# Optimization experiments

Hardware: AMD Instinct MI355X
Metric: run time of the kernel (lower is better)

## Reference

```python
import jax, jax.numpy as jnp
import numpy as np

N, E, DIN, DH, DOUT = 50000, 800000, 128, 256, 128
EPS = 1e-5
SLOPE = 0.01  # torch leaky_relu default


def setup_inputs() -> dict:
    key = jax.random.key(0)
    ks = jax.random.split(key, 8)
    w = lambda k, shape: jax.random.normal(k, shape, jnp.float32) * 0.05
    return {
        "x": jax.random.normal(ks[0], (N, DIN), jnp.float32),
        "edge_index": jax.random.randint(ks[1], (2, E), 0, N, jnp.int32),
        "W0": w(ks[2], (DH, DIN)),  "b0": jnp.zeros((DH,), jnp.float32),
        "g0": jnp.ones((DH,), jnp.float32), "be0": jnp.zeros((DH,), jnp.float32),
        "W1": w(ks[3], (DH, DH)),   "b1": jnp.zeros((DH,), jnp.float32),
        "g1": jnp.ones((DH,), jnp.float32), "be1": jnp.zeros((DH,), jnp.float32),
        "W2": w(ks[4], (DOUT, DH)), "b2": jnp.zeros((DOUT,), jnp.float32),
        "g2": jnp.ones((DOUT,), jnp.float32), "be2": jnp.zeros((DOUT,), jnp.float32),
    }


def _gcn_forward(x, edge_index, params):
    n = x.shape[0]
    loop = jnp.arange(n, dtype=edge_index.dtype)
    src = jnp.concatenate([edge_index[0], loop])  # add self-loops
    dst = jnp.concatenate([edge_index[1], loop])
    deg = jnp.zeros((n,), x.dtype).at[dst].add(1.0)
    dinv = jax.lax.rsqrt(deg)  # deg >= 1 due to self-loops
    enorm = (dinv[src] * dinv[dst])[:, None]  # [E+N, 1]

    def conv(h, W, b):
        h = h @ W.T  # linear first (PyG GCNConv), messages in out_dim
        msg = h[src] * enorm
        return jax.ops.segment_sum(msg, dst, num_segments=n) + b

    def bn(h, g, be):  # BatchNorm1d, training-mode batch stats (biased var)
        mu = h.mean(0)
        var = ((h - mu) ** 2).mean(0)
        return (h - mu) * jax.lax.rsqrt(var + EPS) * g + be

    (W0, b0, g0, be0, W1, b1, g1, be1, W2, b2, g2, be2) = params
    h = jax.nn.leaky_relu(bn(conv(x, W0, b0), g0, be0), SLOPE)
    h = jax.nn.leaky_relu(bn(conv(h, W1, b1), g1, be1), SLOPE)
    h = bn(conv(h, W2, b2), g2, be2)  # last layer: no leaky_relu
    return h


def reference(x, edge_index, W0, b0, g0, be0, W1, b1, g1, be1, W2, b2, g2, be2):
    return _gcn_forward(x, edge_index,
                        (W0, b0, g0, be0, W1, b1, g1, be1, W2, b2, g2, be2))
```

## Files before the change

kernel.cpp:

```cpp
#include <hip/hip_runtime.h>
#include <hip/hip_bf16.h>

#define N_NODES 50000
#define N_EDGES 800000
#define DIN 128
#define DH   256
#define DOUT 128
#define EPSV 1e-5f
#define SLOPE 0.01f
#define SCAN_NB ((N_NODES + 255) / 256)

typedef __bf16 bf16x8 __attribute__((ext_vector_type(8)));
typedef __bf16 bf16x4 __attribute__((ext_vector_type(4)));
typedef float  f32x4  __attribute__((ext_vector_type(4)));

__global__ void cast3_kernel(const float* __restrict__ W0, const float* __restrict__ W1,
                             const float* __restrict__ W2,
                             __bf16* __restrict__ w0b, __bf16* __restrict__ w1b,
                             __bf16* __restrict__ w2b) {
    constexpr int n0 = DH * DIN / 4, n1 = DH * DH / 4, n2 = DOUT * DH / 4;
    int i = blockIdx.x * blockDim.x + threadIdx.x;
    const float* src; __bf16* dst; int k;
    if (i < n0)           { src = W0; dst = w0b; k = i; }
    else if (i < n0 + n1) { src = W1; dst = w1b; k = i - n0; }
    else if (i < n0 + n1 + n2) { src = W2; dst = w2b; k = i - n0 - n1; }
    else return;
    float4 v = ((const float4*)src)[k];
    bf16x4 o; o[0] = (__bf16)v.x; o[1] = (__bf16)v.y; o[2] = (__bf16)v.z; o[3] = (__bf16)v.w;
    ((bf16x4*)dst)[k] = o;
}

__global__ void cast_scale_kernel(const float* __restrict__ src, const float* __restrict__ dinv,
                                  __bf16* __restrict__ dst) {
    int i = blockIdx.x * blockDim.x + threadIdx.x;
    if (i < N_NODES * (DIN / 8)) {
        int row = i / (DIN / 8);
        float d = dinv[row];
        float4 a = ((const float4*)src)[i * 2];
        float4 b = ((const float4*)src)[i * 2 + 1];
        bf16x8 o;
        o[0] = (__bf16)(a.x * d); o[1] = (__bf16)(a.y * d);
        o[2] = (__bf16)(a.z * d); o[3] = (__bf16)(a.w * d);
        o[4] = (__bf16)(b.x * d); o[5] = (__bf16)(b.y * d);
        o[6] = (__bf16)(b.z * d); o[7] = (__bf16)(b.w * d);
        ((bf16x8*)dst)[i] = o;
    }
}

__global__ void deg_kernel(const int* __restrict__ dst, int* __restrict__ deg) {
    int i = blockIdx.x * blockDim.x + threadIdx.x;
    if (i < N_EDGES) atomicAdd(&deg[dst[i]], 1);
}

__global__ __launch_bounds__(256) void scan_bsum(const int* __restrict__ deg,
                                                 int* __restrict__ bsum,
                                                 float* __restrict__ dinv) {
    __shared__ int lds[256];
    int i = blockIdx.x * 256 + threadIdx.x;
    int dv = 0;
    if (i < N_NODES) {
        dv = deg[i] + 1;
        dinv[i] = rsqrtf((float)dv);
    }
    lds[threadIdx.x] = dv;
    __syncthreads();
    #pragma unroll
    for (int off = 128; off > 0; off >>= 1) {
        if (threadIdx.x < off) lds[threadIdx.x] += lds[threadIdx.x + off];
        __syncthreads();
    }
    if (threadIdx.x == 0) bsum[blockIdx.x] = lds[0];
}

__global__ __launch_bounds__(256) void scan_boffs(const int* __restrict__ bsum,
                                                  int* __restrict__ boffs) {
    __shared__ int lds[256];
    const int t = threadIdx.x;
    lds[t] = (t < SCAN_NB) ? bsum[t] : 0;
    __syncthreads();
    #pragma unroll
    for (int off = 1; off < 256; off <<= 1) {
        int add = (t >= off) ? lds[t - off] : 0;
        __syncthreads();
        lds[t] += add;
        __syncthreads();
    }
    boffs[t] = (t == 0) ? 0 : lds[t - 1];
}

__global__ __launch_bounds__(256) void scan_write(const int* __restrict__ deg,
                                                  const int* __restrict__ boffs,
                                                  int* __restrict__ rp) {
    __shared__ int lds[256];
    const int t = threadIdx.x;
    int i = blockIdx.x * 256 + t;
    int v = (i < N_NODES) ? deg[i] + 1 : 0;
    lds[t] = v;
    __syncthreads();
    #pragma unroll
    for (int off = 1; off < 256; off <<= 1) {
        int add = (t >= off) ? lds[t - off] : 0;
        __syncthreads();
        lds[t] += add;
        __syncthreads();
    }
    if (i < N_NODES) rp[i] = boffs[blockIdx.x] + lds[t] - v;
    if (i == N_NODES - 1) rp[N_NODES] = boffs[blockIdx.x] + lds[t];
}

__global__ void scatter_kernel(const int* __restrict__ ei,
                               const int* __restrict__ rp, int* __restrict__ cursor,
                               int* __restrict__ csr) {
    int e = blockIdx.x * blockDim.x + threadIdx.x;
    if (e >= N_EDGES + N_NODES) return;
    int pos, src;
    if (e < N_EDGES) {
        src = ei[e]; int dst = ei[N_EDGES + e];
        pos = rp[dst] + atomicAdd(&cursor[dst], 1);
    } else {
        src = e - N_EDGES;
        pos = rp[src + 1] - 1;
    }
    csr[pos] = src;
}

template<int C8>
__global__ __launch_bounds__(256) void spmm_b(const int* __restrict__ rp,
                                              const int* __restrict__ csr,
                                              const float* __restrict__ dinv,
                                              const __bf16* __restrict__ h,
                                              __bf16* __restrict__ outp) {
    constexpr int RPB = 256 / C8;
    const int r = blockIdx.x * RPB + threadIdx.x / C8;
    const int l = threadIdx.x % C8;
    if (r >= N_NODES) return;
    const bf16x8* __restrict__ h8 = (const bf16x8*)h;
    const int e0 = rp[r], e1 = rp[r + 1];
    float acc0[8] = {}, acc1[8] = {};
    int e = e0;
    for (; e + 8 <= e1; e += 8) {
        int p[8];
        #pragma unroll
        for (int u = 0; u < 8; ++u) p[u] = csr[e + u];
        bf16x8 v[8];
        #pragma unroll
        for (int u = 0; u < 8; ++u) v[u] = h8[(long)p[u] * C8 + l];
        #pragma unroll
        for (int u = 0; u < 8; ++u) {
            #pragma unroll
            for (int j = 0; j < 8; ++j) {
                if (u & 1) acc1[j] += (float)v[u][j];
                else       acc0[j] += (float)v[u][j];
            }
        }
    }
    for (; e + 2 <= e1; e += 2) {
        int p0 = csr[e], p1 = csr[e + 1];
        bf16x8 v0 = h8[(long)p0 * C8 + l];
        bf16x8 v1 = h8[(long)p1 * C8 + l];
        #pragma unroll
        for (int j = 0; j < 8; ++j) {
            acc0[j] += (float)v0[j];
            acc1[j] += (float)v1[j];
        }
    }
    if (e < e1) {
        int p0 = csr[e];
        bf16x8 v0 = h8[(long)p0 * C8 + l];
        #pragma unroll
        for (int j = 0; j < 8; ++j) acc0[j] += (float)v0[j];
    }
    const float d = dinv[r];
    bf16x8 ob;
    #pragma unroll
    for (int j = 0; j < 8; ++j) ob[j] = (__bf16)((acc0[j] + acc1[j]) * d);
    ((bf16x8*)outp)[(long)r * C8 + l] = ob;
}

template<int K, int NC, bool FUSE_BN, bool RELU, bool SCALE>
__global__ __launch_bounds__(256) void gemm_tile(const __bf16* __restrict__ A,
                                                 const __bf16* __restrict__ W,
                                                 const float* __restrict__ ss,
                                                 const float* __restrict__ dinv,
                                                 __bf16* __restrict__ C,
                                                 int M) {
    constexpr int NW = NC / 64;
    constexpr int MW = 4 / NW;
    constexpr int BM = MW * 64;
    constexpr int NSTEP = K / 32;
    __shared__ __bf16 As[2][BM][40];

    const int tid = threadIdx.x;
    const int wave = tid >> 6, lane = tid & 63;
    const int ln15 = lane & 15, kg = lane >> 4;
    const int wm = wave / NW, wn = wave % NW;
    const int m0 = blockIdx.x * BM;
    const int srow = tid >> 2, schunk = tid & 3;

    int grow[MW];
    #pragma unroll
    for (int p = 0; p < MW; ++p) {
        int gr = m0 + p * 64 + srow;
        grow[p] = gr < M ? gr : M - 1;
    }

    f32x4 acc[4][4];
    #pragma unroll
    for (int i = 0; i < 4; ++i)
        #pragma unroll
        for (int j = 0; j < 4; ++j) acc[i][j] = (f32x4){0.f, 0.f, 0.f, 0.f};

#define LOAD_A(vv, kt_)                                                         \
    _Pragma("unroll")                                                           \
    for (int p = 0; p < MW; ++p)                                                \
        vv[p] = *(const bf16x8*)(A + (long)grow[p] * K + (kt_) + schunk * 8);

#define XFORM_A(vv, kt_)                                                        \
    if (FUSE_BN) {                                                              \
        const f32x4* ss4 = (const f32x4*)ss;                                    \
        int ci = ((kt_) + schunk * 8) >> 2;                                     \
        f32x4 sc0 = ss4[ci],            sc1 = ss4[ci + 1];                      \
        f32x4 sh0 = ss4[(K >> 2) + ci], sh1 = ss4[(K >> 2) + ci + 1];           \
        _Pragma("unroll")                                                       \
        for (int p = 0; p < MW; ++p) {                                          \
            float f[8];                                                         \
            _Pragma("unroll")                                                   \
            for (int j = 0; j < 4; ++j) {                                       \
                f[j]     = fmaf((float)vv[p][j],     sc0[j], sh0[j]);           \
                f[j + 4] = fmaf((float)vv[p][j + 4], sc1[j], sh1[j]);           \
            }                                                                   \
            if (RELU) {                                                         \
                _Pragma("unroll")                                               \
                for (int j = 0; j < 8; ++j) f[j] = f[j] > 0.f ? f[j] : SLOPE * f[j]; \
            }                                                                   \
            _Pragma("unroll")                                                   \
            for (int j = 0; j < 8; ++j) vv[p][j] = (__bf16)f[j];                \
        }                                                                       \
    }

#define WRITE_A(buf, vv)                                                        \
    _Pragma("unroll")                                                           \
    for (int p = 0; p < MW; ++p)                                                \
        *(bf16x8*)(&As[buf][p * 64 + srow][schunk * 8]) = vv[p];

    bf16x8 v0[MW], v[MW];
    LOAD_A(v0, 0)
    XFORM_A(v0, 0)
    WRITE_A(0, v0)
    if (NSTEP > 1) {
        LOAD_A(v, 32)
        XFORM_A(v, 32)
    }
    __syncthreads();

    int cur = 0;
    #pragma unroll
    for (int step = 0; step < NSTEP; ++step) {
        const int kt = step * 32;
        if (step + 1 < NSTEP) {
            WRITE_A(cur ^ 1, v)
        }
        bf16x8 vn[MW];
        if (step + 2 < NSTEP) {
            LOAD_A(vn, kt + 64)
        }
        bf16x8 b[4];
        #pragma unroll
        for (int j = 0; j < 4; ++j)
            b[j] = *(const bf16x8*)(W + (long)(wn * 64 + j * 16 + ln15) * K + kt + kg * 8);
        #pragma unroll
        for (int i = 0; i < 4; ++i) {
            bf16x8 a = *(const bf16x8*)(&As[cur][wm * 64 + i * 16 + ln15][kg * 8]);
            #pragma unroll
            for (int j = 0; j < 4; ++j)
                acc[i][j] = __builtin_amdgcn_mfma_f32_16x16x32_bf16(a, b[j], acc[i][j], 0, 0, 0);
        }
        if (step + 2 < NSTEP) {
            XFORM_A(vn, kt + 64)
            #pragma unroll
            for (int p = 0; p < MW; ++p) v[p] = vn[p];
        }
        __syncthreads();
        cur ^= 1;
    }
#undef LOAD_A
#undef XFORM_A
#undef WRITE_A

    #pragma unroll
    for (int i = 0; i < 4; ++i) {
        #pragma unroll
        for (int q = 0; q < 4; ++q) {
            int r = m0 + wm * 64 + i * 16 + kg * 4 + q;
            if (r < M) {
                float d = SCALE ? dinv[r] : 1.0f;
                #pragma unroll
                for (int j = 0; j < 4; ++j)
                    C[(long)r * NC + wn * 64 + j * 16 + ln15] = (__bf16)(acc[i][j][q] * d);
            }
        }
    }
}

#define NB_STATS 128
template<int C>
__global__ __launch_bounds__(256) void bn_stats(const __bf16* __restrict__ hp,
                                                float* __restrict__ partial) {
    constexpr int LPR = C / 4;
    constexpr int RPI = 256 / LPR;
    const int chunk = threadIdx.x % LPR;
    const int rof   = threadIdx.x / LPR;
    float s[4] = {}, s2[4] = {};
    for (int r = blockIdx.x * RPI + rof; r < N_NODES; r += NB_STATS * RPI) {
        bf16x4 x = ((const bf16x4*)hp)[(long)r * LPR + chunk];
        #pragma unroll
        for (int j = 0; j < 4; ++j) {
            float v = (float)x[j];
            s[j] += v; s2[j] += v * v;
        }
    }
    __shared__ float red[256 * 8];
    #pragma unroll
    for (int j = 0; j < 4; ++j) { red[threadIdx.x * 8 + j] = s[j]; red[threadIdx.x * 8 + 4 + j] = s2[j]; }
    __syncthreads();
    if (rof == 0) {
        #pragma unroll
        for (int g = 1; g < RPI; ++g) {
            #pragma unroll
            for (int j = 0; j < 4; ++j) {
                s[j]  += red[(g * LPR + chunk) * 8 + j];
                s2[j] += red[(g * LPR + chunk) * 8 + 4 + j];
            }
        }
        #pragma unroll
        for (int j = 0; j < 4; ++j) {
            partial[blockIdx.x * 2 * C + chunk * 4 + j]     = s[j];
            partial[blockIdx.x * 2 * C + C + chunk * 4 + j] = s2[j];
        }
    }
}

template<int C>
__global__ __launch_bounds__(1024) void bn_reduce(const float* __restrict__ partial, int nb,
                                                  const float* __restrict__ g,
                                                  const float* __restrict__ be,
                                                  float* __restrict__ ss) {
    constexpr int G = 1024 / C;
    const int c = threadIdx.x % C;
    const int grp = threadIdx.x / C;
    float s = 0.f, q = 0.f;
    for (int b = grp; b < nb; b += G) {
        s += partial[(long)b * 2 * C + c];
        q += partial[(long)b * 2 * C + C + c];
    }
    __shared__ float reds[1024], redq[1024];
    reds[threadIdx.x] = s; redq[threadIdx.x] = q;
    __syncthreads();
    if (grp == 0) {
        #pragma unroll
        for (int gg = 1; gg < G; ++gg) { s += reds[gg * C + c]; q += redq[gg * C + c]; }
        const float invn = 1.0f / (float)N_NODES;
        float mean = s * invn;
        float var  = q * invn - mean * mean;
        float rstd = rsqrtf(var + EPSV);
        float sc = g[c] * rstd;
        ss[c] = sc;
        ss[C + c] = be[c] - mean * sc;
    }
}

template<int C>
__global__ __launch_bounds__(256) void bn_apply_b2f(const __bf16* __restrict__ in,
                                                    float* __restrict__ outp,
                                                    const float* __restrict__ ss) {
    constexpr int LPR = C / 4;
    const long total = (long)N_NODES * LPR;
    const long stride = (long)gridDim.x * blockDim.x;
    for (long idx = (long)blockIdx.x * blockDim.x + threadIdx.x; idx < total; idx += stride) {
        int chunk = (int)(idx % LPR);
        float4 sc = ((const float4*)ss)[chunk];
        float4 sh = ((const float4*)(ss + C))[chunk];
        bf16x4 x = ((const bf16x4*)in)[idx];
        float4 o;
        o.x = fmaf((float)x[0], sc.x, sh.x);
        o.y = fmaf((float)x[1], sc.y, sh.y);
        o.z = fmaf((float)x[2], sc.z, sh.z);
        o.w = fmaf((float)x[3], sc.w, sh.w);
        ((float4*)outp)[idx] = o;
    }
}

extern "C" void kernel_launch(void* const* d_in, const int* in_sizes, int n_in,
                              void* d_out, int out_size, void* d_ws, size_t ws_size,
                              hipStream_t stream) {
    const float* x   = (const float*)d_in[0];
    const int*   ei  = (const int*)  d_in[1];
    const float* W0  = (const float*)d_in[2];
    const float* g0  = (const float*)d_in[4];
    const float* be0 = (const float*)d_in[5];
    const float* W1  = (const float*)d_in[6];
    const float* g1  = (const float*)d_in[8];
    const float* be1 = (const float*)d_in[9];
    const float* W2  = (const float*)d_in[10];
    const float* g2  = (const float*)d_in[12];
    const float* be2 = (const float*)d_in[13];
    float* out = (float*)d_out;

    char* wsb = (char*)d_ws;
    auto alloc = [&](size_t bytes) { char* p = wsb; wsb += (bytes + 255) & ~255UL; return p; };
    int*    deg     = (int*)   alloc(N_NODES * 4);
    int*    cursor  = (int*)   alloc(N_NODES * 4);
    int*    rp      = (int*)   alloc((N_NODES + 4) * 4);
    float*  dinv    = (float*) alloc(N_NODES * 4);
    int*    bsum    = (int*)   alloc(256 * 4);
    int*    boffs   = (int*)   alloc(257 * 4);
    float*  partial = (float*) alloc(NB_STATS * 2 * DH * 4);
    float*  ss      = (float*) alloc(2 * DH * 4);
    int*    csr     = (int*)   alloc((size_t)(N_EDGES + N_NODES) * 4);
    __bf16* w0b     = (__bf16*)alloc(DH * DIN * 2);
    __bf16* w1b     = (__bf16*)alloc(DH * DH * 2);
    __bf16* w2b     = (__bf16*)alloc(DOUT * DH * 2);
    __bf16* xb      = (__bf16*)alloc((size_t)N_NODES * DIN * 2);
    __bf16* bf0     = (__bf16*)alloc((size_t)N_NODES * DH * 2);
    __bf16* bf1     = (__bf16*)alloc((size_t)N_NODES * DH * 2);

    hipMemsetAsync(deg, 0, (size_t)((char*)cursor - (char*)deg) + N_NODES * 4, stream);

    cast3_kernel<<<(DH * DIN / 4 + DH * DH / 4 + DOUT * DH / 4 + 255) / 256, 256, 0, stream>>>(
        W0, W1, W2, w0b, w1b, w2b);

    deg_kernel<<<(N_EDGES + 255) / 256, 256, 0, stream>>>(ei + N_EDGES, deg);
    scan_bsum<<<SCAN_NB, 256, 0, stream>>>(deg, bsum, dinv);
    scan_boffs<<<1, 256, 0, stream>>>(bsum, boffs);
    scan_write<<<SCAN_NB, 256, 0, stream>>>(deg, boffs, rp);
    scatter_kernel<<<(N_EDGES + N_NODES + 255) / 256, 256, 0, stream>>>(ei, rp, cursor, csr);

    cast_scale_kernel<<<(N_NODES * (DIN / 8) + 255) / 256, 256, 0, stream>>>(x, dinv, xb);

    spmm_b<DIN / 8><<<(N_NODES * (DIN / 8) + 255) / 256, 256, 0, stream>>>(
        rp, csr, dinv, xb, bf0);
    gemm_tile<DIN, DH, false, false, false><<<(N_NODES + 63) / 64, 256, 0, stream>>>(
        bf0, w0b, nullptr, nullptr, bf1, N_NODES);
    bn_stats<DH><<<NB_STATS, 256, 0, stream>>>(bf1, partial);
    bn_reduce<DH><<<1, 1024, 0, stream>>>(partial, NB_STATS, g0, be0, ss);

    gemm_tile<DH, DH, true, true, true><<<(N_NODES + 63) / 64, 256, 0, stream>>>(
        bf1, w1b, ss, dinv, bf0, N_NODES);
    spmm_b<DH / 8><<<(N_NODES * (DH / 8) + 255) / 256, 256, 0, stream>>>(
        rp, csr, dinv, bf0, bf1);
    bn_stats<DH><<<NB_STATS, 256, 0, stream>>>(bf1, partial);
    bn_reduce<DH><<<1, 1024, 0, stream>>>(partial, NB_STATS, g1, be1, ss);

    gemm_tile<DH, DOUT, true, true, true><<<(N_NODES + 127) / 128, 256, 0, stream>>>(
        bf1, w2b, ss, dinv, bf0, N_NODES);
    spmm_b<DOUT / 8><<<(N_NODES * (DOUT / 8) + 255) / 256, 256, 0, stream>>>(
        rp, csr, dinv, bf0, bf1);
    bn_stats<DOUT><<<NB_STATS, 256, 0, stream>>>(bf1, partial);
    bn_reduce<DOUT><<<1, 1024, 0, stream>>>(partial, NB_STATS, g2, be2, ss);
    bn_apply_b2f<DOUT><<<2048, 256, 0, stream>>>(bf1, out, ss);
}
```

Measured before the change: 407.2 us.

## Build CSR via two-level bucketed scatter with LDS-local placement

Replaces the per-destination global atomic scatter with two passes. The first pass scatters each edge into a 64-node bucket through padded per-bucket atomic cursors, packing the source and the local destination into a temporary array. The second pass places edges into final CSR slots with LDS atomics and also writes the self-loops. The goal is less global atomic contention and more local writes, at the cost of an extra pass over a temporary buffer and two more launches.

```diff
diff --git a/kernel.cpp b/kernel.cpp
--- a/kernel.cpp
+++ b/kernel.cpp
@@ -9,6 +9,7 @@
 #define EPSV 1e-5f
 #define SLOPE 0.01f
 #define SCAN_NB ((N_NODES + 255) / 256)
+#define NBUCKET ((N_NODES + 63) / 64)
 
 typedef __bf16 bf16x8 __attribute__((ext_vector_type(8)));
 typedef __bf16 bf16x4 __attribute__((ext_vector_type(4)));
@@ -108,20 +109,48 @@
     if (i == N_NODES - 1) rp[N_NODES] = boffs[blockIdx.x] + lds[t];
 }
 
-__global__ void scatter_kernel(const int* __restrict__ ei,
-                               const int* __restrict__ rp, int* __restrict__ cursor,
-                               int* __restrict__ csr) {
+__global__ void bcur_init(const int* __restrict__ rp, int* __restrict__ bcur) {
+    int b = blockIdx.x * blockDim.x + threadIdx.x;
+    if (b < NBUCKET) bcur[b * 16] = rp[b * 64];
+}
+
+__global__ void scatter_bucket(const int* __restrict__ ei, int* __restrict__ bcur,
+                               int* __restrict__ tmp) {
     int e = blockIdx.x * blockDim.x + threadIdx.x;
-    if (e >= N_EDGES + N_NODES) return;
-    int pos, src;
-    if (e < N_EDGES) {
-        src = ei[e]; int dst = ei[N_EDGES + e];
-        pos = rp[dst] + atomicAdd(&cursor[dst], 1);
-    } else {
-        src = e - N_EDGES;
-        pos = rp[src + 1] - 1;
-    }
-    csr[pos] = src;
+    if (e >= N_EDGES) return;
+    int src = ei[e], dst = ei[N_EDGES + e];
+    int b = dst >> 6;
+    int pos = atomicAdd(&bcur[b * 16], 1);
+    tmp[pos] = src | ((dst & 63) << 17);
+}
+
+__global__ __launch_bounds__(256) void csr_place(const int* __restrict__ rp,
+                                                 const int* __restrict__ bcur,
+                                                 const int* __restrict__ tmp,
+                                                 int* __restrict__ csr) {
+    __shared__ int lcur[64];
+    __shared__ int lrp[65];
+    const int b = blockIdx.x, t = threadIdx.x;
+    const int node0 = b * 64;
+    if (t < 64) lcur[t] = 0;
+    if (t < 65) {
+        int n = node0 + t;
+        lrp[t] = rp[n <= N_NODES ? n : N_NODES];
+    }
+    __syncthreads();
+    const int estart = lrp[0];
+    const int eend = bcur[b * 16];
+    for (int e = estart + t; e < eend; e += 256) {
+        int v = tmp[e];
+        int src = v & 0x1FFFF;
+        int dl = v >> 17;
+        int slot = lrp[dl] + atomicAdd(&lcur[dl], 1);
+        csr[slot] = src;
+    }
+    if (t < 64) {
+        int n = node0 + t;
+        if (n < N_NODES) csr[lrp[t + 1] - 1] = n;
+    }
 }
 
 template<int C8>
@@ -409,14 +438,15 @@
     char* wsb = (char*)d_ws;
     auto alloc = [&](size_t bytes) { char* p = wsb; wsb += (bytes + 255) & ~255UL; return p; };
     int*    deg     = (int*)   alloc(N_NODES * 4);
-    int*    cursor  = (int*)   alloc(N_NODES * 4);
     int*    rp      = (int*)   alloc((N_NODES + 4) * 4);
     float*  dinv    = (float*) alloc(N_NODES * 4);
     int*    bsum    = (int*)   alloc(256 * 4);
     int*    boffs   = (int*)   alloc(257 * 4);
+    int*    bcur    = (int*)   alloc((size_t)NBUCKET * 16 * 4);
     float*  partial = (float*) alloc(NB_STATS * 2 * DH * 4);
     float*  ss      = (float*) alloc(2 * DH * 4);
     int*    csr     = (int*)   alloc((size_t)(N_EDGES + N_NODES) * 4);
+    int*    tmp     = (int*)   alloc((size_t)(N_EDGES + N_NODES) * 4);
     __bf16* w0b     = (__bf16*)alloc(DH * DIN * 2);
     __bf16* w1b     = (__bf16*)alloc(DH * DH * 2);
     __bf16* w2b     = (__bf16*)alloc(DOUT * DH * 2);
@@ -424,7 +454,7 @@
     __bf16* bf0     = (__bf16*)alloc((size_t)N_NODES * DH * 2);
     __bf16* bf1     = (__bf16*)alloc((size_t)N_NODES * DH * 2);
 
-    hipMemsetAsync(deg, 0, (size_t)((char*)cursor - (char*)deg) + N_NODES * 4, stream);
+    hipMemsetAsync(deg, 0, N_NODES * 4, stream);
 
     cast3_kernel<<<(DH * DIN / 4 + DH * DH / 4 + DOUT * DH / 4 + 255) / 256, 256, 0, stream>>>(
         W0, W1, W2, w0b, w1b, w2b);
@@ -433,7 +463,9 @@
     scan_bsum<<<SCAN_NB, 256, 0, stream>>>(deg, bsum, dinv);
     scan_boffs<<<1, 256, 0, stream>>>(bsum, boffs);
     scan_write<<<SCAN_NB, 256, 0, stream>>>(deg, boffs, rp);
-    scatter_kernel<<<(N_EDGES + N_NODES + 255) / 256, 256, 0, stream>>>(ei, rp, cursor, csr);
+    bcur_init<<<(NBUCKET + 255) / 256, 256, 0, stream>>>(rp, bcur);
+    scatter_bucket<<<(N_EDGES + 255) / 256, 256, 0, stream>>>(ei, bcur, tmp);
+    csr_place<<<NBUCKET, 256, 0, stream>>>(rp, bcur, tmp, csr);
 
     cast_scale_kernel<<<(N_NODES * (DIN / 8) + 255) / 256, 256, 0, stream>>>(x, dinv, xb);
 
```

Result: no change. 407.0 us (-0.0%).
